# Kernel optimization log

Hardware: AMD Instinct MI355X
Metric: run time of the kernel (lower is better)

## Reference

```python
import jax, jax.numpy as jnp
import numpy as np

L, B, T, C, H, V, CTX = 4, 2, 1024, 1024, 16, 50257, 2048
D = C // H
EPS = 1e-5
NEG_SLOPE = 0.01


def layer_norm(x, w, b):
    mu = jnp.mean(x, axis=-1, keepdims=True)
    var = jnp.mean(jnp.square(x - mu), axis=-1, keepdims=True)
    return (x - mu) * jax.lax.rsqrt(var + EPS) * w + b


def setup_inputs() -> dict:
    key = jax.random.key(0)
    ks = jax.random.split(key, 8)
    s = 0.02  # init std as in _init_weights
    return {
        "idx": jax.random.randint(ks[0], (B, T), 0, V),
        "wte": jax.random.normal(ks[1], (V, C), jnp.float32) * s,
        "wpe": jax.random.normal(ks[2], (CTX, C), jnp.float32) * s,
        "ln1_w": jnp.ones((L, C), jnp.float32),
        "ln1_b": jnp.zeros((L, C), jnp.float32),
        "attn_w": jax.random.normal(ks[3], (L, C, 3 * C), jnp.float32) * s,
        "attn_b": jnp.zeros((L, 3 * C), jnp.float32),
        "proj_w": jax.random.normal(ks[4], (L, C, C), jnp.float32) * s,
        "proj_b": jnp.zeros((L, C), jnp.float32),
        "ln2_w": jnp.ones((L, C), jnp.float32),
        "ln2_b": jnp.zeros((L, C), jnp.float32),
        "fc_w": jax.random.normal(ks[5], (L, C, 4 * C), jnp.float32) * s,
        "fc_b": jnp.zeros((L, 4 * C), jnp.float32),
        "fcproj_w": jax.random.normal(ks[6], (L, 4 * C, C), jnp.float32) * s,
        "fcproj_b": jnp.zeros((L, C), jnp.float32),
        "lnf_w": jnp.ones((C,), jnp.float32),
        "lnf_b": jnp.zeros((C,), jnp.float32),
    }


def reference(idx, wte, wpe, ln1_w, ln1_b, attn_w, attn_b, proj_w, proj_b,
              ln2_w, ln2_b, fc_w, fc_b, fcproj_w, fcproj_b, lnf_w, lnf_b):
    t = idx.shape[1]
    x = wte[idx] + wpe[:t]  # [B,T,C]; dropout=0 => identity
    causal = jnp.tril(jnp.ones((t, t), bool))  # [T,T]
    scale = 1.0 / np.sqrt(D)
    for l in range(L):
        # --- causal self-attention ---
        h = layer_norm(x, ln1_w[l], ln1_b[l])
        qkv = h @ attn_w[l] + attn_b[l]  # [B,T,3C]
        q, k, v = jnp.split(qkv, 3, axis=-1)
        q = q.reshape(B, t, H, D)
        k = k.reshape(B, t, H, D)
        v = v.reshape(B, t, H, D)
        att = jnp.einsum('bthd,bshd->bhts', q, k) * scale  # [B,H,T,T]
        att = jnp.where(causal, att, -jnp.inf)
        att = jax.nn.softmax(att, axis=-1)
        y = jnp.einsum('bhts,bshd->bthd', att, v).reshape(B, t, C)
        x = x + y @ proj_w[l] + proj_b[l]
        # --- MLP ---
        h = layer_norm(x, ln2_w[l], ln2_b[l])
        h = h @ fc_w[l] + fc_b[l]
        h = jnp.where(h >= 0, h, NEG_SLOPE * h)  # LeakyReLU(0.01)
        x = x + h @ fcproj_w[l] + fcproj_b[l]
    x = layer_norm(x, lnf_w, lnf_b)
    # targets=None path: lm_head on last position only, tied weight = wte
    logits = x[:, -1:, :] @ wte.T  # [B,1,V]
    return logits
```

## Files before the change

kernel.cpp:

```cpp
#include <hip/hip_runtime.h>
#include <hip/hip_bf16.h>


#define TT 1024
#define CC 1024
#define NHEAD 16
#define DHEAD 64
#define NBATCH 2
#define VOCAB 50257

typedef __attribute__((ext_vector_type(8))) short bf16x8;
typedef __attribute__((ext_vector_type(4))) float f32x4;

#define GPTR(p) (const __attribute__((address_space(1))) void*)(p)
#define LPTR(p) (__attribute__((address_space(3))) void*)(p)

__device__ __forceinline__ unsigned short f2bf(float f) {
  union { float f; unsigned u; } v; v.f = f;
  unsigned r = v.u + 0x7fffu + ((v.u >> 16) & 1u);
  return (unsigned short)(r >> 16);
}
__device__ __forceinline__ float bf2f(unsigned short u) {
  union { unsigned u; float f; } v; v.u = ((unsigned)u) << 16;
  return v.f;
}

__device__ __forceinline__ f32x4 mfma_bf16(bf16x8 a, bf16x8 b, f32x4 c) {
  return __builtin_amdgcn_mfma_f32_16x16x32_bf16(a, b, c, 0, 0, 0);
}

__global__ __launch_bounds__(256) void embed_k(const int* __restrict__ idx,
    const float* __restrict__ wte, const float* __restrict__ wpe,
    float* __restrict__ x)
{
  int row = blockIdx.x;
  int t = row & (TT - 1);
  int tok = idx[row];
  const float4* a = (const float4*)(wte + (size_t)tok * CC);
  const float4* p = (const float4*)(wpe + (size_t)t * CC);
  float4* o = (float4*)(x + (size_t)row * CC);
  int i = threadIdx.x;
  float4 va = a[i], vp = p[i];
  o[i] = make_float4(va.x + vp.x, va.y + vp.y, va.z + vp.z, va.w + vp.w);
}

__device__ __forceinline__ unsigned pk2(float lo, float hi) {
  return (unsigned)f2bf(lo) | ((unsigned)f2bf(hi) << 16);
}

__global__ __launch_bounds__(256) void ln_k(const float* __restrict__ x,
    const float* __restrict__ w, const float* __restrict__ b,
    unsigned short* __restrict__ out)
{
  int row = blockIdx.x * 4 + (threadIdx.x >> 6);
  int lane = threadIdx.x & 63;
  const float* xr = x + (size_t)row * CC + lane * 16;
  float4 v[4];
  float s = 0.f, ss = 0.f;
#pragma unroll
  for (int i = 0; i < 4; ++i) {
    v[i] = *(const float4*)(xr + i * 4);
    s  += v[i].x + v[i].y + v[i].z + v[i].w;
    ss += v[i].x*v[i].x + v[i].y*v[i].y + v[i].z*v[i].z + v[i].w*v[i].w;
  }
#pragma unroll
  for (int off = 1; off < 64; off <<= 1) {
    s  += __shfl_xor(s, off, 64);
    ss += __shfl_xor(ss, off, 64);
  }
  float mu = s * (1.f / CC);
  float var = ss * (1.f / CC) - mu * mu;
  float rstd = rsqrtf(var + 1e-5f);
  const float* wr = w + lane * 16;
  const float* br = b + lane * 16;
  unsigned q[8];
#pragma unroll
  for (int i = 0; i < 4; ++i) {
    float4 wv = *(const float4*)(wr + i * 4);
    float4 bv = *(const float4*)(br + i * 4);
    float o0 = (v[i].x - mu) * rstd * wv.x + bv.x;
    float o1 = (v[i].y - mu) * rstd * wv.y + bv.y;
    float o2 = (v[i].z - mu) * rstd * wv.z + bv.z;
    float o3 = (v[i].w - mu) * rstd * wv.w + bv.w;
    q[i*2+0] = pk2(o0, o1);
    q[i*2+1] = pk2(o2, o3);
  }
  uint4* op = (uint4*)(out + (size_t)row * CC + lane * 16);
  op[0] = make_uint4(q[0], q[1], q[2], q[3]);
  op[1] = make_uint4(q[4], q[5], q[6], q[7]);
}

__global__ void lnrow_k(const float* __restrict__ x,
    const float* __restrict__ w, const float* __restrict__ b,
    float* __restrict__ outv)
{
  int row = blockIdx.x;
  int lane = threadIdx.x;
  const float* xr = x + ((size_t)(row * TT + (TT - 1))) * CC + lane * 16;
  float4 v[4];
  float s = 0.f, ss = 0.f;
#pragma unroll
  for (int i = 0; i < 4; ++i) {
    v[i] = *(const float4*)(xr + i * 4);
    s  += v[i].x + v[i].y + v[i].z + v[i].w;
    ss += v[i].x*v[i].x + v[i].y*v[i].y + v[i].z*v[i].z + v[i].w*v[i].w;
  }
#pragma unroll
  for (int off = 1; off < 64; off <<= 1) {
    s  += __shfl_xor(s, off, 64);
    ss += __shfl_xor(ss, off, 64);
  }
  float mu = s * (1.f / CC);
  float var = ss * (1.f / CC) - mu * mu;
  float rstd = rsqrtf(var + 1e-5f);
  float* op = outv + (size_t)row * CC + lane * 16;
  const float* wr = w + lane * 16;
  const float* br = b + lane * 16;
#pragma unroll
  for (int i = 0; i < 4; ++i) {
    float4 wv = *(const float4*)(wr + i * 4);
    float4 bv = *(const float4*)(br + i * 4);
    float4 o;
    o.x = (v[i].x - mu) * rstd * wv.x + bv.x;
    o.y = (v[i].y - mu) * rstd * wv.y + bv.y;
    o.z = (v[i].z - mu) * rstd * wv.z + bv.z;
    o.w = (v[i].w - mu) * rstd * wv.w + bv.w;
    *(float4*)(op + i * 4) = o;
  }
}

__global__ __launch_bounds__(256) void wconv_k(const float* __restrict__ W,
    unsigned short* __restrict__ Wt, int K, int N)
{
  const size_t lo = (size_t)blockIdx.z * K * N;
  __shared__ float tile[64][65];
  const int k0 = blockIdx.x << 6;
  const int n0 = blockIdx.y << 6;
  const int t = threadIdx.x;
  {
    const int r = t >> 4, c4 = t & 15;
#pragma unroll
    for (int p = 0; p < 4; ++p) {
      int kr = r + (p << 4);
      float4 v = *(const float4*)(W + lo + (size_t)(k0 + kr) * N + n0 + (c4 << 2));
      tile[kr][(c4 << 2) + 0] = v.x;
      tile[kr][(c4 << 2) + 1] = v.y;
      tile[kr][(c4 << 2) + 2] = v.z;
      tile[kr][(c4 << 2) + 3] = v.w;
    }
  }
  __syncthreads();
  {
    const int n = t >> 2, kq = t & 3;
    bf16x8 o0, o1;
#pragma unroll
    for (int e = 0; e < 8; ++e) o0[e] = (short)f2bf(tile[(kq << 4) + e][n]);
#pragma unroll
    for (int e = 0; e < 8; ++e) o1[e] = (short)f2bf(tile[(kq << 4) + 8 + e][n]);
    unsigned short* dst = Wt + lo + (size_t)(n0 + n) * K + k0 + (kq << 4);
    *(bf16x8*)dst = o0;
    *(bf16x8*)(dst + 8) = o1;
  }
}

#define MODE_QKV  0
#define MODE_PART 1
#define MODE_FC   2

template<int MODE>
__global__ __launch_bounds__(256) void gemm_k(
    const unsigned short* __restrict__ A,
    const unsigned short* __restrict__ Wt,
    const float* __restrict__ bias,
    float* __restrict__ pbuf,
    unsigned short* __restrict__ obf,
    unsigned short* __restrict__ q_o,
    unsigned short* __restrict__ k_o,
    unsigned short* __restrict__ v_o,
    int M, int N, int K, int kchunk, int ncol0)
{
  __shared__ alignas(16) unsigned short Asm[128 * 64];
  __shared__ alignas(16) unsigned short Bsm[128 * 64];
  const int tid  = threadIdx.x;
  const int wave = tid >> 6, lane = tid & 63;
  const int lg = lane >> 4, ll = lane & 15;
  const int nTM = M >> 7, nTN = N >> 7;
  int bid = blockIdx.x;
  const int mt = bid % nTM; bid /= nTM;
  const int nt = bid % nTN;
  const int s  = bid / nTN;
  const int m0 = mt << 7, n0 = nt << 7;
  const int kb = s * kchunk, ke = kb + kchunk;
  const int wm = (wave >> 1) << 6, wn = (wave & 1) << 6;
  f32x4 acc[4][4] = {};

  for (int k0 = kb; k0 < ke; k0 += 64) {
#pragma unroll
    for (int c = 0; c < 4; ++c) {
      const int seg = (wave << 2) + c;
      const int g = (seg << 6) + lane;
      const int row = g >> 3, kq = g & 7;
      const unsigned short* asrc = A  + (size_t)(m0 + row) * K + k0 + (kq << 3);
      const unsigned short* bsrc = Wt + (size_t)(n0 + row) * K + k0 + (kq << 3);
      unsigned short* adst = Asm + (size_t)(seg << 9);
      unsigned short* bdst = Bsm + (size_t)(seg << 9);
      __builtin_amdgcn_global_load_lds(GPTR(asrc), LPTR(adst), 16, 0, 0);
      __builtin_amdgcn_global_load_lds(GPTR(bsrc), LPTR(bdst), 16, 0, 0);
    }
    __syncthreads();
#pragma unroll
    for (int kk = 0; kk < 2; ++kk) {
      bf16x8 af[4], bfr[4];
#pragma unroll
      for (int i = 0; i < 4; ++i)
        af[i] = *(const bf16x8*)(Asm + ((wm + i * 16 + ll) << 6) + (kk << 5) + (lg << 3));
#pragma unroll
      for (int j = 0; j < 4; ++j)
        bfr[j] = *(const bf16x8*)(Bsm + ((wn + j * 16 + ll) << 6) + (kk << 5) + (lg << 3));
#pragma unroll
      for (int i = 0; i < 4; ++i)
#pragma unroll
        for (int j = 0; j < 4; ++j)
          acc[i][j] = mfma_bf16(af[i], bfr[j], acc[i][j]);
    }
    __syncthreads();
  }

#pragma unroll
  for (int j = 0; j < 4; ++j) {
    int gc = n0 + wn + j * 16 + ll;
    int gcol = ncol0 + gc;
    float bv = (MODE == MODE_PART) ? 0.f : bias[gcol];
#pragma unroll
    for (int i = 0; i < 4; ++i) {
      int gr0 = m0 + wm + i * 16 + (lg << 2);
#pragma unroll
      for (int r = 0; r < 4; ++r) {
        int grow = gr0 + r;
        float val = acc[i][j][r] + bv;
        if (MODE == MODE_QKV) {
          int which = gcol >> 10;
          int head = (gcol >> 6) & 15;
          int d = gcol & 63;
          int bb = grow >> 10, t = grow & (TT - 1);
          unsigned short* dst = (which == 0) ? q_o : (which == 1) ? k_o : v_o;
          dst[(((size_t)((bb << 4) + head)) << 16) + ((size_t)t << 6) + d] = f2bf(val);
        } else if (MODE == MODE_FC) {
          val = (val >= 0.f) ? val : 0.01f * val;
          obf[(size_t)grow * N + gc] = f2bf(val);
        } else {
          pbuf[((size_t)s * M + grow) * N + gc] = val;
        }
      }
    }
  }
}

__global__ __launch_bounds__(256) void reduce_k(float* __restrict__ x,
    const float* __restrict__ P, const float* __restrict__ bias,
    int N4, int total4, int splits)
{
  const float4* P4 = (const float4*)P;
  const float4* b4 = (const float4*)bias;
  float4* x4 = (float4*)x;
  int stride = gridDim.x * 256;
  for (int i = blockIdx.x * 256 + threadIdx.x; i < total4; i += stride) {
    float4 s = b4[i & (N4 - 1)];
    for (int sp = 0; sp < splits; ++sp) {
      float4 p = P4[(size_t)sp * total4 + i];
      s.x += p.x; s.y += p.y; s.z += p.z; s.w += p.w;
    }
    float4 xv = x4[i];
    x4[i] = make_float4(xv.x + s.x, xv.y + s.y, xv.z + s.z, xv.w + s.w);
  }
}

__global__ __launch_bounds__(256) void attn_k(
    const unsigned short* __restrict__ Qb,
    const unsigned short* __restrict__ Kb,
    const unsigned short* __restrict__ Vb,
    unsigned short* __restrict__ ybuf)
{
  __shared__ alignas(16) unsigned short Ksm[64][72];
  __shared__ alignas(16) unsigned short Vtsm[64][64];
  __shared__ alignas(16) unsigned short Psm[4][16][72];
  const int tid = threadIdx.x;
  const int wave = tid >> 6, lane = tid & 63;
  const int lg = lane >> 4, ll = lane & 15;
  const int qt = blockIdx.x & 15, bh = blockIdx.x >> 4;
  const int b = bh >> 4, h = bh & 15;
  const size_t base = (size_t)bh << 16;
  const int q0 = qt << 6;

  const int qrow = q0 + wave * 16 + ll;
  bf16x8 aq0 = *(const bf16x8*)(Qb + base + ((size_t)qrow << 6) + (lg << 3));
  bf16x8 aq1 = *(const bf16x8*)(Qb + base + ((size_t)qrow << 6) + 32 + (lg << 3));

  f32x4 accy[4] = {};
  float m_run[4], l_run[4];
#pragma unroll
  for (int r = 0; r < 4; ++r) { m_run[r] = -1e30f; l_run[r] = 0.f; }

  const int sk_row = tid >> 3, sk_cq = tid & 7;
  const int sv_d = tid & 63, sv_kq = tid >> 6;
  const int qg0 = q0 + wave * 16 + (lg << 2);

  for (int kb = 0; kb <= qt; ++kb) {
    const int kbase = kb << 6;
#pragma unroll
    for (int p = 0; p < 2; ++p) {
      int r = sk_row + (p << 5);
      bf16x8 kv = *(const bf16x8*)(Kb + base + ((size_t)(kbase + r) << 6) + (sk_cq << 3));
      *(bf16x8*)&Ksm[r][sk_cq << 3] = kv;
    }
#pragma unroll
    for (int p = 0; p < 2; ++p) {
      int kq8 = sv_kq + (p << 2);
      bf16x8 wv;
#pragma unroll
      for (int e = 0; e < 8; ++e)
        wv[e] = (short)Vb[base + ((size_t)(kbase + (kq8 << 3) + e) << 6) + sv_d];
      int u = kq8 ^ (sv_d & 7);
      *(bf16x8*)&Vtsm[sv_d][u << 3] = wv;
    }
    __syncthreads();

    float p_[4][4];
    float rmax[4] = {-1e30f, -1e30f, -1e30f, -1e30f};
#pragma unroll
    for (int kk = 0; kk < 4; ++kk) {
      f32x4 z = {};
      bf16x8 bk0 = *(const bf16x8*)&Ksm[kk * 16 + ll][lg << 3];
      bf16x8 bk1 = *(const bf16x8*)&Ksm[kk * 16 + ll][32 + (lg << 3)];
      z = mfma_bf16(aq0, bk0, z);
      z = mfma_bf16(aq1, bk1, z);
      int key = kbase + kk * 16 + ll;
#pragma unroll
      for (int r = 0; r < 4; ++r) {
        float v = z[r] * 0.125f;
        v = (key > qg0 + r) ? -1e30f : v;
        p_[kk][r] = v;
        rmax[r] = fmaxf(rmax[r], v);
      }
    }
#pragma unroll
    for (int off = 1; off < 16; off <<= 1)
#pragma unroll
      for (int r = 0; r < 4; ++r)
        rmax[r] = fmaxf(rmax[r], __shfl_xor(rmax[r], off, 64));

    float alpha[4], rsum[4];
#pragma unroll
    for (int r = 0; r < 4; ++r) {
      float mn = fmaxf(m_run[r], rmax[r]);
      alpha[r] = __expf(m_run[r] - mn);
      m_run[r] = mn;
      rsum[r] = 0.f;
    }
#pragma unroll
    for (int kk = 0; kk < 4; ++kk)
#pragma unroll
      for (int r = 0; r < 4; ++r) {
        float e = __expf(p_[kk][r] - m_run[r]);
        p_[kk][r] = e;
        rsum[r] += e;
      }
#pragma unroll
    for (int off = 1; off < 16; off <<= 1)
#pragma unroll
      for (int r = 0; r < 4; ++r)
        rsum[r] += __shfl_xor(rsum[r], off, 64);
#pragma unroll
    for (int r = 0; r < 4; ++r)
      l_run[r] = l_run[r] * alpha[r] + rsum[r];
#pragma unroll
    for (int df = 0; df < 4; ++df)
#pragma unroll
      for (int r = 0; r < 4; ++r)
        accy[df][r] *= alpha[r];

#pragma unroll
    for (int kk = 0; kk < 4; ++kk)
#pragma unroll
      for (int r = 0; r < 4; ++r)
        Psm[wave][(lg << 2) + r][kk * 16 + ll] = f2bf(p_[kk][r]);
    bf16x8 pa0 = *(const bf16x8*)&Psm[wave][ll][lg << 3];
    bf16x8 pa1 = *(const bf16x8*)&Psm[wave][ll][32 + (lg << 3)];

#pragma unroll
    for (int df = 0; df < 4; ++df) {
      int d = df * 16 + ll;
      int u0 = lg ^ (d & 7);
      int u1 = (4 + lg) ^ (d & 7);
      bf16x8 bv0 = *(const bf16x8*)&Vtsm[d][u0 << 3];
      bf16x8 bv1 = *(const bf16x8*)&Vtsm[d][u1 << 3];
      accy[df] = mfma_bf16(pa0, bv0, accy[df]);
      accy[df] = mfma_bf16(pa1, bv1, accy[df]);
    }
    __syncthreads();
  }

#pragma unroll
  for (int df = 0; df < 4; ++df)
#pragma unroll
    for (int r = 0; r < 4; ++r) {
      int qr = qg0 + r;
      float y = accy[df][r] / l_run[r];
      ybuf[(((size_t)((b << 10) + qr)) << 10) + (h << 6) + df * 16 + ll] = f2bf(y);
    }
}

__global__ __launch_bounds__(256) void gemv_k(const float* __restrict__ W,
    int ldw, const float* __restrict__ xv, int K,
    float* __restrict__ part, int N)
{
  __shared__ float xs[2][128];
  const int tid = threadIdx.x;
  const int n = blockIdx.x * 256 + tid;
  const int ks = blockIdx.y;
  if (tid < 128) xs[0][tid] = xv[ks * 128 + tid];
  else           xs[1][tid - 128] = xv[K + ks * 128 + (tid - 128)];
  __syncthreads();
  float a0 = 0.f, a1 = 0.f;
  const float* wp = W + (size_t)(ks * 128) * ldw + n;
#pragma unroll 4
  for (int k = 0; k < 128; ++k) {
    float w = wp[(size_t)k * ldw];
    a0 += xs[0][k] * w;
    a1 += xs[1][k] * w;
  }
  part[((size_t)ks * 2 + 0) * N + n] = a0;
  part[((size_t)ks * 2 + 1) * N + n] = a1;
}

#define MG_PLAIN 0
#define MG_LEAKY 1
#define MG_ADDX  2
template<int MG>
__global__ __launch_bounds__(256) void gmerge_k(const float* __restrict__ part,
    const float* __restrict__ bias, float* __restrict__ outp, int N, int KT)
{
  int n = blockIdx.x * 256 + threadIdx.x;
#pragma unroll
  for (int b = 0; b < 2; ++b) {
    float s = bias[n];
    for (int ks = 0; ks < KT; ++ks)
      s += part[((size_t)ks * 2 + b) * N + n];
    if (MG == MG_PLAIN) outp[(size_t)b * N + n] = s;
    else if (MG == MG_LEAKY) outp[(size_t)b * N + n] = (s >= 0.f) ? s : 0.01f * s;
    else x_add: outp[((size_t)(b * TT + TT - 1)) * CC + n] += s;
  }
}

__global__ __launch_bounds__(256) void attnlast_k(
    const float* __restrict__ q_last,
    const unsigned short* __restrict__ Kb,
    const unsigned short* __restrict__ Vb,
    float* __restrict__ apart)
{
  __shared__ float qs[64];
  __shared__ float wm[4], wl[4], wacc[4][64];
  const int tid = threadIdx.x;
  const int wave = tid >> 6, lane = tid & 63;
  const int bh = blockIdx.x, ks = blockIdx.y;
  const int b = bh >> 4, h = bh & 15;
  const size_t base = (size_t)bh << 16;
  const int key = ks * 256 + wave * 64 + lane;

  if (tid < 64) qs[tid] = q_last[b * CC + h * 64 + tid];
  __syncthreads();

  float s = 0.f;
  const unsigned short* kp = Kb + base + ((size_t)key << 6);
#pragma unroll
  for (int o = 0; o < 8; ++o) {
    bf16x8 kv = *(const bf16x8*)(kp + (o << 3));
#pragma unroll
    for (int e = 0; e < 8; ++e)
      s += qs[(o << 3) + e] * bf2f((unsigned short)kv[e]);
  }
  s *= 0.125f;
  float m = s;
#pragma unroll
  for (int off = 1; off < 64; off <<= 1)
    m = fmaxf(m, __shfl_xor(m, off, 64));
  float p = __expf(s - m);
  float l = p;
#pragma unroll
  for (int off = 1; off < 64; off <<= 1)
    l += __shfl_xor(l, off, 64);

  float acc = 0.f;
  const unsigned short* vp = Vb + base + ((size_t)(ks * 256 + wave * 64) << 6);
  for (int j = 0; j < 64; ++j) {
    float pj = __shfl(p, j, 64);
    acc += pj * bf2f(vp[((size_t)j << 6) + lane]);
  }
  if (lane == 0) { wm[wave] = m; wl[wave] = l; }
  wacc[wave][lane] = acc;
  __syncthreads();
  if (wave == 0) {
    float m0 = fmaxf(fmaxf(wm[0], wm[1]), fmaxf(wm[2], wm[3]));
    float lt = 0.f, at = 0.f;
#pragma unroll
    for (int sI = 0; sI < 4; ++sI) {
      float f = __expf(wm[sI] - m0);
      lt += wl[sI] * f;
      at += wacc[sI][lane] * f;
    }
    float* op = apart + ((size_t)bh * 4 + ks) * 66;
    if (lane == 0) { op[0] = m0; op[1] = lt; }
    op[2 + lane] = at;
  }
}

__global__ void attnmerge_k(const float* __restrict__ apart,
    float* __restrict__ y_last)
{
  const int bh = blockIdx.x, lane = threadIdx.x;
  const int b = bh >> 4, h = bh & 15;
  const float* p0 = apart + (size_t)bh * 4 * 66;
  float m0 = fmaxf(fmaxf(p0[0], p0[66]), fmaxf(p0[132], p0[198]));
  float lt = 0.f, at = 0.f;
#pragma unroll
  for (int s = 0; s < 4; ++s) {
    const float* ps = p0 + s * 66;
    float f = __expf(ps[0] - m0);
    lt += ps[1] * f;
    at += ps[2 + lane] * f;
  }
  y_last[b * CC + h * 64 + lane] = at / lt;
}

__global__ __launch_bounds__(256) void head_k(const float* __restrict__ xf,
    const float* __restrict__ wte, float* __restrict__ out)
{
  int v = (blockIdx.x << 2) + (threadIdx.x >> 6);
  if (v >= VOCAB) return;
  int lane = threadIdx.x & 63;
  const float4* wr = (const float4*)(wte + (size_t)v * CC);
  const float4* x0 = (const float4*)xf;
  const float4* x1 = (const float4*)(xf + CC);
  float a0 = 0.f, a1 = 0.f;
#pragma unroll
  for (int i = 0; i < 4; ++i) {
    float4 wv = wr[lane + i * 64];
    float4 p0 = x0[lane + i * 64];
    float4 p1 = x1[lane + i * 64];
    a0 += wv.x * p0.x + wv.y * p0.y + wv.z * p0.z + wv.w * p0.w;
    a1 += wv.x * p1.x + wv.y * p1.y + wv.z * p1.z + wv.w * p1.w;
  }
#pragma unroll
  for (int off = 1; off < 64; off <<= 1) {
    a0 += __shfl_xor(a0, off, 64);
    a1 += __shfl_xor(a1, off, 64);
  }
  if (lane == 0) {
    out[v] = a0;
    out[VOCAB + v] = a1;
  }
}

extern "C" void kernel_launch(void* const* d_in, const int* in_sizes, int n_in,
                              void* d_out, int out_size, void* d_ws, size_t ws_size,
                              hipStream_t stream)
{
  const int*   idx      = (const int*)d_in[0];
  const float* wte      = (const float*)d_in[1];
  const float* wpe      = (const float*)d_in[2];
  const float* ln1_w    = (const float*)d_in[3];
  const float* ln1_b    = (const float*)d_in[4];
  const float* attn_w   = (const float*)d_in[5];
  const float* attn_b   = (const float*)d_in[6];
  const float* proj_w   = (const float*)d_in[7];
  const float* proj_b   = (const float*)d_in[8];
  const float* ln2_w    = (const float*)d_in[9];
  const float* ln2_b    = (const float*)d_in[10];
  const float* fc_w     = (const float*)d_in[11];
  const float* fc_b     = (const float*)d_in[12];
  const float* fcproj_w = (const float*)d_in[13];
  const float* fcproj_b = (const float*)d_in[14];
  const float* lnf_w    = (const float*)d_in[15];
  const float* lnf_b    = (const float*)d_in[16];
  float* out = (float*)d_out;

  const size_t MB = 1u << 20;
  char* ws = (char*)d_ws;
  float*          x   = (float*)ws;
  unsigned short* h   = (unsigned short*)(ws + 8*MB);
  unsigned short* qb  = (unsigned short*)(ws + 12*MB);
  unsigned short* kb_ = (unsigned short*)(ws + 16*MB);
  unsigned short* vb  = (unsigned short*)(ws + 20*MB);
  unsigned short* yb  = (unsigned short*)(ws + 24*MB);
  unsigned short* hf  = (unsigned short*)(ws + 28*MB);
  char* sm = ws + 44*MB;
  float* xf     = (float*)(sm + 0);
  float* xs1    = (float*)(sm + 16*1024);
  float* xs2    = (float*)(sm + 32*1024);
  float* ylast  = (float*)(sm + 48*1024);
  float* qlast  = (float*)(sm + 64*1024);
  float* hlast  = (float*)(sm + 80*1024);
  float* gpart  = (float*)(sm + 128*1024);
  float* apart  = (float*)(sm + 512*1024);
  unsigned short* wt_attn   = (unsigned short*)(ws + 46*MB);
  unsigned short* wt_proj   = (unsigned short*)(ws + 70*MB);
  unsigned short* wt_fc     = (unsigned short*)(ws + 76*MB);
  unsigned short* wt_fcproj = (unsigned short*)(ws + 100*MB);
  float*          Ppart     = (float*)(ws + 124*MB);

  embed_k<<<NBATCH * TT, 256, 0, stream>>>(idx, wte, wpe, x);

  wconv_k<<<dim3(16, 48, 4), 256, 0, stream>>>(attn_w, wt_attn, 1024, 3072);
  wconv_k<<<dim3(16, 16, 3), 256, 0, stream>>>(proj_w, wt_proj, 1024, 1024);
  wconv_k<<<dim3(16, 64, 3), 256, 0, stream>>>(fc_w, wt_fc, 1024, 4096);
  wconv_k<<<dim3(64, 16, 3), 256, 0, stream>>>(fcproj_w, wt_fcproj, 4096, 1024);

  for (int l = 0; l < 3; ++l) {
    ln_k<<<512, 256, 0, stream>>>(x, ln1_w + l * CC, ln1_b + l * CC, h);
    gemm_k<MODE_QKV><<<16 * 24, 256, 0, stream>>>(h,
        wt_attn + (size_t)l * 3072 * 1024, attn_b + (size_t)l * 3 * CC,
        nullptr, nullptr, qb, kb_, vb, 2048, 3072, 1024, 1024, 0);
    attn_k<<<NBATCH * NHEAD * 16, 256, 0, stream>>>(qb, kb_, vb, yb);
    gemm_k<MODE_PART><<<16 * 8 * 4, 256, 0, stream>>>(yb,
        wt_proj + (size_t)l * 1024 * 1024, nullptr,
        Ppart, nullptr, nullptr, nullptr, nullptr, 2048, 1024, 1024, 256, 0);
    reduce_k<<<512, 256, 0, stream>>>(x, Ppart, proj_b + l * CC, 256, 2048 * 256, 4);
    ln_k<<<512, 256, 0, stream>>>(x, ln2_w + l * CC, ln2_b + l * CC, h);
    gemm_k<MODE_FC><<<16 * 32, 256, 0, stream>>>(h,
        wt_fc + (size_t)l * 1024 * 4096, fc_b + (size_t)l * 4 * CC,
        nullptr, hf, nullptr, nullptr, nullptr, 2048, 4096, 1024, 1024, 0);
    gemm_k<MODE_PART><<<16 * 8 * 8, 256, 0, stream>>>(hf,
        wt_fcproj + (size_t)l * 4096 * 1024, nullptr,
        Ppart, nullptr, nullptr, nullptr, nullptr, 2048, 1024, 4096, 512, 0);
    reduce_k<<<512, 256, 0, stream>>>(x, Ppart, fcproj_b + l * CC, 256, 2048 * 256, 8);
  }

  {
    const int l = 3;
    ln_k<<<512, 256, 0, stream>>>(x, ln1_w + l * CC, ln1_b + l * CC, h);
    gemm_k<MODE_QKV><<<16 * 16, 256, 0, stream>>>(h,
        wt_attn + (size_t)l * 3072 * 1024 + (size_t)1024 * 1024,
        attn_b + (size_t)l * 3 * CC,
        nullptr, nullptr, qb, kb_, vb, 2048, 2048, 1024, 1024, 1024);
    lnrow_k<<<2, 64, 0, stream>>>(x, ln1_w + l * CC, ln1_b + l * CC, xs1);
    gemv_k<<<dim3(4, 8), 256, 0, stream>>>(attn_w + (size_t)l * CC * 3 * CC,
        3072, xs1, 1024, gpart, 1024);
    gmerge_k<MG_PLAIN><<<4, 256, 0, stream>>>(gpart, attn_b + (size_t)l * 3 * CC,
        qlast, 1024, 8);
    attnlast_k<<<dim3(32, 4), 256, 0, stream>>>(qlast, kb_, vb, apart);
    attnmerge_k<<<32, 64, 0, stream>>>(apart, ylast);
    gemv_k<<<dim3(4, 8), 256, 0, stream>>>(proj_w + (size_t)l * CC * CC,
        1024, ylast, 1024, gpart, 1024);
    gmerge_k<MG_ADDX><<<4, 256, 0, stream>>>(gpart, proj_b + l * CC, x, 1024, 8);
    lnrow_k<<<2, 64, 0, stream>>>(x, ln2_w + l * CC, ln2_b + l * CC, xs2);
    gemv_k<<<dim3(16, 8), 256, 0, stream>>>(fc_w + (size_t)l * CC * 4 * CC,
        4096, xs2, 1024, gpart, 4096);
    gmerge_k<MG_LEAKY><<<16, 256, 0, stream>>>(gpart, fc_b + (size_t)l * 4 * CC,
        hlast, 4096, 8);
    gemv_k<<<dim3(4, 32), 256, 0, stream>>>(fcproj_w + (size_t)l * 4 * CC * CC,
        1024, hlast, 4096, gpart, 1024);
    gmerge_k<MG_ADDX><<<4, 256, 0, stream>>>(gpart, fcproj_b + l * CC, x, 1024, 32);
  }

  lnrow_k<<<2, 64, 0, stream>>>(x, lnf_w, lnf_b, xf);
  head_k<<<(VOCAB + 3) / 4, 256, 0, stream>>>(xf, wte, out);
}
```

Before: 778.3 us.

## Fuse split-K reduction with layernorm and double-buffer GEMM LDS tiles

Replaces the separate split-K reduce kernel and following layernorm with a single redln_k that adds bias and partials to the residual and emits the bf16 normalized rows, cutting a full pass over x and one launch per use. The GEMM now double-buffers its LDS tiles so the next K-slice loads overlap the MFMA work, with one barrier per iteration instead of two. The fc-proj split-K factor drops from 8 to 4, reducing partial-buffer traffic but also halving the grid size. The larger LDS footprint (64KB) may lower occupancy.

Result: faster. 726.2 us (-6.7%).

```diff
diff --git a/kernel.cpp b/kernel.cpp
--- a/kernel.cpp
+++ b/kernel.cpp
@@ -86,6 +86,68 @@
     q[i*2+1] = pk2(o2, o3);
   }
   uint4* op = (uint4*)(out + (size_t)row * CC + lane * 16);
+  op[0] = make_uint4(q[0], q[1], q[2], q[3]);
+  op[1] = make_uint4(q[4], q[5], q[6], q[7]);
+}
+
+__global__ __launch_bounds__(256) void redln_k(float* __restrict__ x,
+    const float* __restrict__ P, const float* __restrict__ bias,
+    const float* __restrict__ lw, const float* __restrict__ lb,
+    unsigned short* __restrict__ out, int splits)
+{
+  int row = blockIdx.x * 4 + (threadIdx.x >> 6);
+  int lane = threadIdx.x & 63;
+  const int c0 = lane * 16;
+  float* xw = x + (size_t)row * CC + c0;
+  float4 v[4];
+#pragma unroll
+  for (int i = 0; i < 4; ++i) v[i] = *(const float4*)(xw + i * 4);
+  {
+    const float4* b4 = (const float4*)(bias + c0);
+#pragma unroll
+    for (int i = 0; i < 4; ++i) {
+      float4 bv = b4[i];
+      v[i].x += bv.x; v[i].y += bv.y; v[i].z += bv.z; v[i].w += bv.w;
+    }
+  }
+  for (int sp = 0; sp < splits; ++sp) {
+    const float4* p4 = (const float4*)(P + ((size_t)sp * 2048 + row) * CC + c0);
+#pragma unroll
+    for (int i = 0; i < 4; ++i) {
+      float4 pv = p4[i];
+      v[i].x += pv.x; v[i].y += pv.y; v[i].z += pv.z; v[i].w += pv.w;
+    }
+  }
+  float s = 0.f, ss = 0.f;
+#pragma unroll
+  for (int i = 0; i < 4; ++i) {
+    *(float4*)(xw + i * 4) = v[i];
+    s  += v[i].x + v[i].y + v[i].z + v[i].w;
+    ss += v[i].x*v[i].x + v[i].y*v[i].y + v[i].z*v[i].z + v[i].w*v[i].w;
+  }
+#pragma unroll
+  for (int off = 1; off < 64; off <<= 1) {
+    s  += __shfl_xor(s, off, 64);
+    ss += __shfl_xor(ss, off, 64);
+  }
+  float mu = s * (1.f / CC);
+  float var = ss * (1.f / CC) - mu * mu;
+  float rstd = rsqrtf(var + 1e-5f);
+  const float* wr = lw + c0;
+  const float* br = lb + c0;
+  unsigned q[8];
+#pragma unroll
+  for (int i = 0; i < 4; ++i) {
+    float4 wv = *(const float4*)(wr + i * 4);
+    float4 bv = *(const float4*)(br + i * 4);
+    float o0 = (v[i].x - mu) * rstd * wv.x + bv.x;
+    float o1 = (v[i].y - mu) * rstd * wv.y + bv.y;
+    float o2 = (v[i].z - mu) * rstd * wv.z + bv.z;
+    float o3 = (v[i].w - mu) * rstd * wv.w + bv.w;
+    q[i*2+0] = pk2(o0, o1);
+    q[i*2+1] = pk2(o2, o3);
+  }
+  uint4* op = (uint4*)(out + (size_t)row * CC + c0);
   op[0] = make_uint4(q[0], q[1], q[2], q[3]);
   op[1] = make_uint4(q[4], q[5], q[6], q[7]);
 }
@@ -179,8 +241,8 @@
     unsigned short* __restrict__ v_o,
     int M, int N, int K, int kchunk, int ncol0)
 {
-  __shared__ alignas(16) unsigned short Asm[128 * 64];
-  __shared__ alignas(16) unsigned short Bsm[128 * 64];
+  __shared__ alignas(16) unsigned short Asm[2][128 * 64];
+  __shared__ alignas(16) unsigned short Bsm[2][128 * 64];
   const int tid  = threadIdx.x;
   const int wave = tid >> 6, lane = tid & 63;
   const int lg = lane >> 4, ll = lane & 15;
@@ -190,41 +252,51 @@
   const int nt = bid % nTN;
   const int s  = bid / nTN;
   const int m0 = mt << 7, n0 = nt << 7;
-  const int kb = s * kchunk, ke = kb + kchunk;
+  const int kb = s * kchunk;
+  const int nIter = kchunk >> 6;
   const int wm = (wave >> 1) << 6, wn = (wave & 1) << 6;
   f32x4 acc[4][4] = {};
 
-  for (int k0 = kb; k0 < ke; k0 += 64) {
-#pragma unroll
-    for (int c = 0; c < 4; ++c) {
-      const int seg = (wave << 2) + c;
-      const int g = (seg << 6) + lane;
-      const int row = g >> 3, kq = g & 7;
-      const unsigned short* asrc = A  + (size_t)(m0 + row) * K + k0 + (kq << 3);
-      const unsigned short* bsrc = Wt + (size_t)(n0 + row) * K + k0 + (kq << 3);
-      unsigned short* adst = Asm + (size_t)(seg << 9);
-      unsigned short* bdst = Bsm + (size_t)(seg << 9);
-      __builtin_amdgcn_global_load_lds(GPTR(asrc), LPTR(adst), 16, 0, 0);
-      __builtin_amdgcn_global_load_lds(GPTR(bsrc), LPTR(bdst), 16, 0, 0);
-    }
+  const int grow_ = ((wave << 8) + lane) >> 3;
+#define STAGE(BUF, K0)                                                        \
+  {                                                                           \
+    _Pragma("unroll")                                                         \
+    for (int c = 0; c < 4; ++c) {                                             \
+      const int seg = (wave << 2) + c;                                        \
+      const int g = (seg << 6) + lane;                                        \
+      const int row = g >> 3, kq = g & 7;                                     \
+      const unsigned short* asrc = A  + (size_t)(m0 + row) * K + (K0) + (kq << 3); \
+      const unsigned short* bsrc = Wt + (size_t)(n0 + row) * K + (K0) + (kq << 3); \
+      __builtin_amdgcn_global_load_lds(GPTR(asrc), LPTR(&Asm[BUF][seg << 9]), 16, 0, 0); \
+      __builtin_amdgcn_global_load_lds(GPTR(bsrc), LPTR(&Bsm[BUF][seg << 9]), 16, 0, 0); \
+    }                                                                         \
+  }
+
+  STAGE(0, kb);
+  int cur = 0;
+  for (int t = 0; t < nIter; ++t) {
     __syncthreads();
+    if (t + 1 < nIter) STAGE(cur ^ 1, kb + ((t + 1) << 6));
+    const unsigned short* As = &Asm[cur][0];
+    const unsigned short* Bs = &Bsm[cur][0];
 #pragma unroll
     for (int kk = 0; kk < 2; ++kk) {
       bf16x8 af[4], bfr[4];
 #pragma unroll
       for (int i = 0; i < 4; ++i)
-        af[i] = *(const bf16x8*)(Asm + ((wm + i * 16 + ll) << 6) + (kk << 5) + (lg << 3));
+        af[i] = *(const bf16x8*)(As + ((wm + i * 16 + ll) << 6) + (kk << 5) + (lg << 3));
 #pragma unroll
       for (int j = 0; j < 4; ++j)
-        bfr[j] = *(const bf16x8*)(Bsm + ((wn + j * 16 + ll) << 6) + (kk << 5) + (lg << 3));
+        bfr[j] = *(const bf16x8*)(Bs + ((wn + j * 16 + ll) << 6) + (kk << 5) + (lg << 3));
 #pragma unroll
       for (int i = 0; i < 4; ++i)
 #pragma unroll
         for (int j = 0; j < 4; ++j)
           acc[i][j] = mfma_bf16(af[i], bfr[j], acc[i][j]);
     }
-    __syncthreads();
-  }
+    cur ^= 1;
+  }
+#undef STAGE
 
 #pragma unroll
   for (int j = 0; j < 4; ++j) {
@@ -256,25 +328,6 @@
   }
 }
 
-__global__ __launch_bounds__(256) void reduce_k(float* __restrict__ x,
-    const float* __restrict__ P, const float* __restrict__ bias,
-    int N4, int total4, int splits)
-{
-  const float4* P4 = (const float4*)P;
-  const float4* b4 = (const float4*)bias;
-  float4* x4 = (float4*)x;
-  int stride = gridDim.x * 256;
-  for (int i = blockIdx.x * 256 + threadIdx.x; i < total4; i += stride) {
-    float4 s = b4[i & (N4 - 1)];
-    for (int sp = 0; sp < splits; ++sp) {
-      float4 p = P4[(size_t)sp * total4 + i];
-      s.x += p.x; s.y += p.y; s.z += p.z; s.w += p.w;
-    }
-    float4 xv = x4[i];
-    x4[i] = make_float4(xv.x + s.x, xv.y + s.y, xv.z + s.z, xv.w + s.w);
-  }
-}
-
 __global__ __launch_bounds__(256) void attn_k(
     const unsigned short* __restrict__ Qb,
     const unsigned short* __restrict__ Kb,
@@ -448,7 +501,7 @@
       s += part[((size_t)ks * 2 + b) * N + n];
     if (MG == MG_PLAIN) outp[(size_t)b * N + n] = s;
     else if (MG == MG_LEAKY) outp[(size_t)b * N + n] = (s >= 0.f) ? s : 0.01f * s;
-    else x_add: outp[((size_t)(b * TT + TT - 1)) * CC + n] += s;
+    else outp[((size_t)(b * TT + TT - 1)) * CC + n] += s;
   }
 }
 
@@ -615,8 +668,9 @@
   wconv_k<<<dim3(16, 64, 3), 256, 0, stream>>>(fc_w, wt_fc, 1024, 4096);
   wconv_k<<<dim3(64, 16, 3), 256, 0, stream>>>(fcproj_w, wt_fcproj, 4096, 1024);
 
+  ln_k<<<512, 256, 0, stream>>>(x, ln1_w, ln1_b, h);
+
   for (int l = 0; l < 3; ++l) {
-    ln_k<<<512, 256, 0, stream>>>(x, ln1_w + l * CC, ln1_b + l * CC, h);
     gemm_k<MODE_QKV><<<16 * 24, 256, 0, stream>>>(h,
         wt_attn + (size_t)l * 3072 * 1024, attn_b + (size_t)l * 3 * CC,
         nullptr, nullptr, qb, kb_, vb, 2048, 3072, 1024, 1024, 0);
@@ -624,20 +678,20 @@
     gemm_k<MODE_PART><<<16 * 8 * 4, 256, 0, stream>>>(yb,
         wt_proj + (size_t)l * 1024 * 1024, nullptr,
         Ppart, nullptr, nullptr, nullptr, nullptr, 2048, 1024, 1024, 256, 0);
-    reduce_k<<<512, 256, 0, stream>>>(x, Ppart, proj_b + l * CC, 256, 2048 * 256, 4);
-    ln_k<<<512, 256, 0, stream>>>(x, ln2_w + l * CC, ln2_b + l * CC, h);
+    redln_k<<<512, 256, 0, stream>>>(x, Ppart, proj_b + l * CC,
+        ln2_w + l * CC, ln2_b + l * CC, h, 4);
     gemm_k<MODE_FC><<<16 * 32, 256, 0, stream>>>(h,
         wt_fc + (size_t)l * 1024 * 4096, fc_b + (size_t)l * 4 * CC,
         nullptr, hf, nullptr, nullptr, nullptr, 2048, 4096, 1024, 1024, 0);
-    gemm_k<MODE_PART><<<16 * 8 * 8, 256, 0, stream>>>(hf,
+    gemm_k<MODE_PART><<<16 * 8 * 4, 256, 0, stream>>>(hf,
         wt_fcproj + (size_t)l * 4096 * 1024, nullptr,
-        Ppart, nullptr, nullptr, nullptr, nullptr, 2048, 1024, 4096, 512, 0);
-    reduce_k<<<512, 256, 0, stream>>>(x, Ppart, fcproj_b + l * CC, 256, 2048 * 256, 8);
+        Ppart, nullptr, nullptr, nullptr, nullptr, 2048, 1024, 4096, 1024, 0);
+    redln_k<<<512, 256, 0, stream>>>(x, Ppart, fcproj_b + l * CC,
+        ln1_w + (l + 1) * CC, ln1_b + (l + 1) * CC, h, 4);
   }
 
   {
     const int l = 3;
-    ln_k<<<512, 256, 0, stream>>>(x, ln1_w + l * CC, ln1_b + l * CC, h);
     gemm_k<MODE_QKV><<<16 * 16, 256, 0, stream>>>(h,
         wt_attn + (size_t)l * 3072 * 1024 + (size_t)1024 * 1024,
         attn_b + (size_t)l * 3 * CC,
```
